# Optimization experiments

Hardware: AMD Instinct MI355X
Metric: run time of the kernel (lower is better)

## Reference

```python
import jax, jax.numpy as jnp
import numpy as np

B, C, H, W_SP = 32, 128, 56, 56
OC, K, STRIDE, PAD = 256, 3, 1, 1


def setup_inputs() -> dict:
    key = jax.random.key(0)
    k1, k2, k3 = jax.random.split(key, 3)
    x = jax.random.normal(k1, (B, C, H, W_SP), dtype=jnp.float32)
    # nn.Linear weight: [out_features, in_features] = [OC, C*K*K]
    W = jax.random.normal(k2, (OC, C * K * K), dtype=jnp.float32) * 0.02
    b = jax.random.normal(k3, (OC,), dtype=jnp.float32) * 0.02
    return {"x": x, "W": W, "b": b}


def reference(x, W, b):
    # The torch module does im2col (unfold+permute+reshape) then Linear.
    # Patch layout after view/permute is (C, kh, kw) flattened, so the
    # Linear weight reshaped to [OC, C, K, K] is exactly an OIHW conv
    # kernel; direct convolution computes identical math without
    # materializing the im2col tensor.
    kernel = W.reshape(OC, C, K, K)
    out = jax.lax.conv_general_dilated(
        x, kernel,
        window_strides=(STRIDE, STRIDE),
        padding=[(PAD, PAD), (PAD, PAD)],
        dimension_numbers=("NCHW", "OIHW", "NCHW"),
    )
    return out + b[None, :, None, None]
```

## Files before the change

kernel.cpp:

```cpp
#include <hip/hip_runtime.h>
#include <hip/hip_bf16.h>
#include <stdint.h>

typedef unsigned short u16;
typedef unsigned int   u32;
typedef __bf16 bf16x8 __attribute__((ext_vector_type(8)));
typedef float  f32x4  __attribute__((ext_vector_type(4)));

#define BATCH 32
#define CIN   128
#define HH    56
#define WW    56
#define OC    256
#define HP    58
#define WP    58
#define PLANE  (HH*WW)
#define KDIM   1152
#define NKT    36

#define XPAD_ELEMS (BATCH*HP*WP*CIN)
#define W3_ELEMS   (OC*KDIM)

#define GLDS16(g, l) __builtin_amdgcn_global_load_lds( \
    (const __attribute__((address_space(1))) void*)(g), \
    (__attribute__((address_space(3))) void*)(l), 16, 0, 0)

__global__ void zero_border(uint4* __restrict__ xp4) {
    int i = blockIdx.x * 256 + threadIdx.x;
    if (i >= 64 * 928) return;
    int row = i / 928;
    int off = i - row * 928;
    int b = row >> 1;
    int h = (row & 1) ? (HP - 1) : 0;
    xp4[((size_t)(b * HP + h) * WP * CIN) / 8 + off] = (uint4){0, 0, 0, 0};
}

__global__ __launch_bounds__(256) void pad_tr(const float* __restrict__ x,
                                              u16* __restrict__ xpad) {
    __shared__ u16 T16[56 * 130];
    const int h = blockIdx.x;
    const int b = blockIdx.y;
    const int tid = threadIdx.x;

    const float* src = x + (size_t)b * CIN * PLANE + h * WW;
#pragma unroll
    for (int j = 0; j < 28; ++j) {
        int flat = j * 256 + tid;
        int c = flat / 56;
        int w = flat - c * 56;
        float v = src[(size_t)c * PLANE + w];
        __hip_bfloat16 bv = __float2bfloat16(v);
        T16[w * 130 + c] = *(u16*)&bv;
    }
    __syncthreads();

    const u32* T32 = (const u32*)T16;
    uint4* dst = (uint4*)(xpad + (size_t)(b * HP + h + 1) * WP * CIN);
#pragma unroll
    for (int j = 0; j < 4; ++j) {
        int g = j * 256 + tid;
        if (g < 928) {
            int wp = g >> 4, cq = g & 15;
            uint4 v = (uint4){0, 0, 0, 0};
            if (wp >= 1 && wp <= 56) {
                int w = wp - 1;
                v.x = T32[w * 65 + cq * 4 + 0];
                v.y = T32[w * 65 + cq * 4 + 1];
                v.z = T32[w * 65 + cq * 4 + 2];
                v.w = T32[w * 65 + cq * 4 + 3];
            }
            dst[g] = v;
        }
    }
}

__global__ void pack_w(const float* __restrict__ W, u16* __restrict__ w3) {
    int o = blockIdx.x * blockDim.x + threadIdx.x;
    if (o >= W3_ELEMS) return;
    int nt   = o / (NKT * 4096);
    int rem  = o - nt * (NKT * 4096);
    int kt   = rem / 4096;
    int rem2 = rem - kt * 4096;
    int ni   = rem2 >> 5;
    int ci   = rem2 & 31;
    int n = nt * 128 + ni;
    int r = kt >> 2;
    int c = ((kt & 3) << 5) + ci;
    float val = W[n * KDIM + c * 9 + r];
    __hip_bfloat16 bv = __float2bfloat16(val);
    w3[o] = *(u16*)&bv;
}

__global__ __launch_bounds__(256) void conv_main(
    const u16* __restrict__ xpad,
    const u16* __restrict__ w3,
    const float* __restrict__ bias,
    float* __restrict__ out)
{
    __shared__ __align__(16) u16 As[2][128 * 32];
    __shared__ __align__(16) u16 Bs[2][128 * 32];

    const int tid  = threadIdx.x;
    const int lane = tid & 63;
    const int wv   = tid >> 6;
    const int m0   = blockIdx.x * 128;
    const int nt   = blockIdx.y;

    const int srow = lane >> 2;
    const int sc   = lane & 3;
    size_t abase[2], bbase[2];
#pragma unroll
    for (int i = 0; i < 2; ++i) {
        int rowid = wv * 32 + i * 16 + srow;
        int q = (sc - ((rowid >> 1) & 3)) & 3;
        abase[i] = (size_t)rowid * 64 + q * 16;
        int m  = m0 + rowid;
        int bb = m / PLANE;
        int s  = m - bb * PLANE;
        int hh = s / WW;
        int ww = s - hh * WW;
        bbase[i] = ((size_t)((bb * HP + hh) * WP + ww) * CIN) * 2 + q * 16;
    }
    const char* w3t = (const char*)(w3 + (size_t)nt * (NKT * 4096));
    const char* xb  = (const char*)xpad;
    char* AsW[2] = { (char*)As[0] + wv * 2048, (char*)As[1] + wv * 2048 };
    char* BsW[2] = { (char*)Bs[0] + wv * 2048, (char*)Bs[1] + wv * 2048 };

    const int wn = wv >> 1, wm = wv & 1;
    const int l16 = lane & 15, quad = lane >> 4;

    int aoff[4], boff[4];
#pragma unroll
    for (int f = 0; f < 4; ++f) {
        int ra = wn * 64 + f * 16 + l16;
        aoff[f] = ra * 64 + ((quad + (ra >> 1)) & 3) * 16;
        int rb = wm * 64 + f * 16 + l16;
        boff[f] = rb * 64 + ((quad + (rb >> 1)) & 3) * 16;
    }

    f32x4 acc[4][4];
#pragma unroll
    for (int f = 0; f < 4; ++f) {
        f32x4 bv = *(const f32x4*)&bias[nt * 128 + wn * 64 + f * 16 + quad * 4];
#pragma unroll
        for (int g = 0; g < 4; ++g) acc[f][g] = bv;
    }

    auto issue = [&](int kt) {
        const int buf = kt & 1;
        const int r  = kt >> 2;
        const int cc = kt & 3;
        const int kh = r / 3;
        const int kw = r - kh * 3;
        const size_t xoff = ((size_t)(kh * WP + kw) * CIN + cc * 32) * 2;
#pragma unroll
        for (int i = 0; i < 2; ++i) {
            GLDS16(w3t + (size_t)kt * 8192 + abase[i], AsW[buf] + i * 1024);
            GLDS16(xb + bbase[i] + xoff,               BsW[buf] + i * 1024);
        }
    };

    issue(0);
#pragma unroll
    for (int kt = 0; kt < NKT; ++kt) {
        __syncthreads();
        if (kt + 1 < NKT) issue(kt + 1);

        const char* Ab = (const char*)As[kt & 1];
        const char* Bb = (const char*)Bs[kt & 1];
        bf16x8 af[4], bfr[4];
#pragma unroll
        for (int f = 0; f < 4; ++f)
            af[f] = *(const bf16x8*)(Ab + aoff[f]);
#pragma unroll
        for (int g = 0; g < 4; ++g)
            bfr[g] = *(const bf16x8*)(Bb + boff[g]);

#pragma unroll
        for (int f = 0; f < 4; ++f)
#pragma unroll
            for (int g = 0; g < 4; ++g)
                acc[f][g] = __builtin_amdgcn_mfma_f32_16x16x32_bf16(
                    af[f], bfr[g], acc[f][g], 0, 0, 0);
    }

    const int n0 = nt * 128 + wn * 64;
#pragma unroll
    for (int g = 0; g < 4; ++g) {
        const int mm = m0 + wm * 64 + g * 16 + l16;
        const int bb = mm / PLANE;
        const int ss = mm - bb * PLANE;
        float* obase = out + (size_t)bb * (OC * PLANE) + ss;
#pragma unroll
        for (int f = 0; f < 4; ++f) {
#pragma unroll
            for (int i = 0; i < 4; ++i) {
                const int n = n0 + f * 16 + quad * 4 + i;
                obase[(size_t)n * PLANE] = acc[f][g][i];
            }
        }
    }
}

extern "C" void kernel_launch(void* const* d_in, const int* in_sizes, int n_in,
                              void* d_out, int out_size, void* d_ws, size_t ws_size,
                              hipStream_t stream) {
    const float* x    = (const float*)d_in[0];
    const float* W    = (const float*)d_in[1];
    const float* bias = (const float*)d_in[2];
    float* out = (float*)d_out;

    u16* xpad = (u16*)d_ws;
    u16* w3   = xpad + XPAD_ELEMS;

    zero_border<<<232, 256, 0, stream>>>((uint4*)xpad);
    pad_tr<<<dim3(HH, BATCH), 256, 0, stream>>>(x, xpad);
    pack_w<<<(W3_ELEMS + 255) / 256, 256, 0, stream>>>(W, w3);

    dim3 grid(784, 2);
    conv_main<<<grid, 256, 0, stream>>>(xpad, w3, bias, out);
}
```

Measured before the change: 215.1 us.

## Load GEMM fragments directly from global into registers, dropping LDS staging

The conv main loop no longer stages A and B tiles through LDS with global_load_lds and barriers. Each wave now loads its own MFMA fragments straight from global memory into a register double buffer. Block indices are also remapped to interleave M tiles across groups of eight, and launch bounds request three blocks per CU. This removes the LDS round trip and the __syncthreads calls, at the cost of redundant global/L2 traffic because the two waves sharing a tile each load it, more register pressure, and uncoalesced 16-byte loads.

```diff
diff --git a/kernel.cpp b/kernel.cpp
--- a/kernel.cpp
+++ b/kernel.cpp
@@ -20,10 +20,6 @@
 
 #define XPAD_ELEMS (BATCH*HP*WP*CIN)
 #define W3_ELEMS   (OC*KDIM)
-
-#define GLDS16(g, l) __builtin_amdgcn_global_load_lds( \
-    (const __attribute__((address_space(1))) void*)(g), \
-    (__attribute__((address_space(3))) void*)(l), 16, 0, 0)
 
 __global__ void zero_border(uint4* __restrict__ xp4) {
     int i = blockIdx.x * 256 + threadIdx.x;
@@ -91,52 +87,40 @@
     w3[o] = *(u16*)&bv;
 }
 
-__global__ __launch_bounds__(256) void conv_main(
+__global__ __launch_bounds__(256, 3) void conv_main(
     const u16* __restrict__ xpad,
     const u16* __restrict__ w3,
     const float* __restrict__ bias,
     float* __restrict__ out)
 {
-    __shared__ __align__(16) u16 As[2][128 * 32];
-    __shared__ __align__(16) u16 Bs[2][128 * 32];
-
     const int tid  = threadIdx.x;
     const int lane = tid & 63;
     const int wv   = tid >> 6;
-    const int m0   = blockIdx.x * 128;
+    const int bx   = blockIdx.x;
+    const int m0   = ((bx & 7) * 98 + (bx >> 3)) * 128;
     const int nt   = blockIdx.y;
 
-    const int srow = lane >> 2;
-    const int sc   = lane & 3;
-    size_t abase[2], bbase[2];
-#pragma unroll
-    for (int i = 0; i < 2; ++i) {
-        int rowid = wv * 32 + i * 16 + srow;
-        int q = (sc - ((rowid >> 1) & 3)) & 3;
-        abase[i] = (size_t)rowid * 64 + q * 16;
-        int m  = m0 + rowid;
+    const int wn = wv >> 1, wm = wv & 1;
+    const int l16 = lane & 15, quad = lane >> 4;
+
+    int aoff[4];
+#pragma unroll
+    for (int f = 0; f < 4; ++f)
+        aoff[f] = (wn * 64 + f * 16 + l16) * 64 + quad * 16;
+
+    size_t rowoff[4];
+#pragma unroll
+    for (int g = 0; g < 4; ++g) {
+        int m  = m0 + wm * 64 + g * 16 + l16;
         int bb = m / PLANE;
         int s  = m - bb * PLANE;
         int hh = s / WW;
         int ww = s - hh * WW;
-        bbase[i] = ((size_t)((bb * HP + hh) * WP + ww) * CIN) * 2 + q * 16;
-    }
+        rowoff[g] = ((size_t)((bb * HP + hh) * WP + ww) * CIN) * 2 + quad * 16;
+    }
+
     const char* w3t = (const char*)(w3 + (size_t)nt * (NKT * 4096));
     const char* xb  = (const char*)xpad;
-    char* AsW[2] = { (char*)As[0] + wv * 2048, (char*)As[1] + wv * 2048 };
-    char* BsW[2] = { (char*)Bs[0] + wv * 2048, (char*)Bs[1] + wv * 2048 };
-
-    const int wn = wv >> 1, wm = wv & 1;
-    const int l16 = lane & 15, quad = lane >> 4;
-
-    int aoff[4], boff[4];
-#pragma unroll
-    for (int f = 0; f < 4; ++f) {
-        int ra = wn * 64 + f * 16 + l16;
-        aoff[f] = ra * 64 + ((quad + (ra >> 1)) & 3) * 16;
-        int rb = wm * 64 + f * 16 + l16;
-        boff[f] = rb * 64 + ((quad + (rb >> 1)) & 3) * 16;
-    }
 
     f32x4 acc[4][4];
 #pragma unroll
@@ -146,42 +130,36 @@
         for (int g = 0; g < 4; ++g) acc[f][g] = bv;
     }
 
-    auto issue = [&](int kt) {
-        const int buf = kt & 1;
+    uint4 Ar[2][4], Br[2][4];
+    auto loadk = [&](int s, int kt) {
+        const char* ab = w3t + (size_t)kt * 8192;
+#pragma unroll
+        for (int f = 0; f < 4; ++f)
+            Ar[s][f] = *(const uint4*)(ab + aoff[f]);
         const int r  = kt >> 2;
-        const int cc = kt & 3;
         const int kh = r / 3;
         const int kw = r - kh * 3;
-        const size_t xoff = ((size_t)(kh * WP + kw) * CIN + cc * 32) * 2;
-#pragma unroll
-        for (int i = 0; i < 2; ++i) {
-            GLDS16(w3t + (size_t)kt * 8192 + abase[i], AsW[buf] + i * 1024);
-            GLDS16(xb + bbase[i] + xoff,               BsW[buf] + i * 1024);
+        const char* bb = xb + ((size_t)(kh * WP + kw) * CIN + (kt & 3) * 32) * 2;
+#pragma unroll
+        for (int g = 0; g < 4; ++g)
+            Br[s][g] = *(const uint4*)(bb + rowoff[g]);
+    };
+
+    loadk(0, 0);
+#pragma unroll
+    for (int kt = 0; kt < NKT; ++kt) {
+        const int cur = kt & 1;
+        if (kt + 1 < NKT) loadk(cur ^ 1, kt + 1);
+#pragma unroll
+        for (int f = 0; f < 4; ++f) {
+            union { uint4 u; bf16x8 b; } av; av.u = Ar[cur][f];
+#pragma unroll
+            for (int g = 0; g < 4; ++g) {
+                union { uint4 u; bf16x8 b; } bvu; bvu.u = Br[cur][g];
+                acc[f][g] = __builtin_amdgcn_mfma_f32_16x16x32_bf16(
+                    av.b, bvu.b, acc[f][g], 0, 0, 0);
+            }
         }
-    };
-
-    issue(0);
-#pragma unroll
-    for (int kt = 0; kt < NKT; ++kt) {
-        __syncthreads();
-        if (kt + 1 < NKT) issue(kt + 1);
-
-        const char* Ab = (const char*)As[kt & 1];
-        const char* Bb = (const char*)Bs[kt & 1];
-        bf16x8 af[4], bfr[4];
-#pragma unroll
-        for (int f = 0; f < 4; ++f)
-            af[f] = *(const bf16x8*)(Ab + aoff[f]);
-#pragma unroll
-        for (int g = 0; g < 4; ++g)
-            bfr[g] = *(const bf16x8*)(Bb + boff[g]);
-
-#pragma unroll
-        for (int f = 0; f < 4; ++f)
-#pragma unroll
-            for (int g = 0; g < 4; ++g)
-                acc[f][g] = __builtin_amdgcn_mfma_f32_16x16x32_bf16(
-                    af[f], bfr[g], acc[f][g], 0, 0, 0);
     }
 
     const int n0 = nt * 128 + wn * 64;
```

New measurement: 336.8 us. 56.6% more time.
